# Optimization experiments

Measured on AMD Instinct MI355X. Metric: run time of the kernel, lower is better.

The kernel has to match this reference:

```python
import jax, jax.numpy as jnp
import numpy as np

B, S, D, E = 2, 2048, 1024, 16  # batch, cutoff (seq), dmodel, n_experts


def setup_inputs() -> dict:
    key = jax.random.key(0)
    k = jax.random.split(key, 6)
    scale = 1.0 / np.sqrt(D)
    return {
        "x": jax.random.normal(k[0], (B, S, D), dtype=jnp.float32),
        "gate": jax.random.normal(k[1], (D, E), dtype=jnp.float32) * scale,
        "W1": jax.random.normal(k[2], (E, D, D), dtype=jnp.float32) * scale,  # lin1: Linear(dmodel, dmodel*E), split per expert
        "b1": jnp.zeros((E, D), dtype=jnp.float32),
        "W2": jax.random.normal(k[3], (E, D, D), dtype=jnp.float32) * scale,  # lin2: Linear(dmodel*E, dmodel), split per expert
        "b2": jnp.zeros((D,), dtype=jnp.float32),
        "topk": 256,
    }


def reference(x, gate, W1, b1, W2, b2, topk):
    # Expert-choice gating: softmax over the token (cutoff) axis per expert.
    logits = jnp.einsum("bsd,de->bse", x, gate)            # (B, S, E)
    probs = jax.nn.softmax(logits, axis=1)                  # softmax over tokens
    # Each expert selects its top-k tokens.
    g, idx = jax.lax.top_k(jnp.swapaxes(probs, 1, 2), topk)  # (B, E, k)
    # Gather selected tokens: (B, E, k, D)
    xin = jnp.take_along_axis(x[:, None, :, :], idx[..., None], axis=2)
    # Per-expert 2-layer FFN (hidden size = dmodel, per width = dmodel*n_experts)
    h = jax.nn.relu(jnp.einsum("bekd,edf->bekf", xin, W1) + b1[None, :, None, :])
    out = jnp.einsum("bekf,efd->bekd", h, W2) + b2           # (B, E, k, D)
    weighted = out * g[..., None]
    # Scatter-add back to token positions.
    y = jnp.zeros_like(x)
    b_idx = jnp.arange(x.shape[0])[:, None, None]            # (B, 1, 1)
    y = y.at[b_idx, idx].add(weighted)
    return y
```

## Files before the change

### kernel.cpp

```cpp
#include <hip/hip_runtime.h>
#include <stdint.h>
#include <math.h>

constexpr int CB = 2;
constexpr int CS = 2048;
constexpr int CD = 1024;
constexpr int CE = 16;
constexpr int CK = 256;

typedef short bf16x8 __attribute__((ext_vector_type(8)));
typedef float f32x4 __attribute__((ext_vector_type(4)));

typedef __attribute__((address_space(3))) unsigned short lds_us;

__device__ __forceinline__ bf16x8 ds_read128(const lds_us* p) {
    bf16x8 v;
    asm volatile("ds_read_b128 %0, %1" : "=v"(v) : "v"(p));
    return v;
}

__device__ inline unsigned short f2bf(float f) {
    union { float f; uint32_t u; } v; v.f = f;
    uint32_t u = v.u;
    uint32_t r = (u + 0x7FFFu + ((u >> 16) & 1u)) >> 16;
    return (unsigned short)r;
}

__global__ __launch_bounds__(256)
void logits_part_kernel(const float* __restrict__ x,
                        const float* __restrict__ gate,
                        float* __restrict__ part,
                        float* __restrict__ y) {
    const int tt = blockIdx.x;
    const int dt = blockIdx.y;
    const int tid = threadIdx.x;

    {
        const int bb = dt * 16 + tt;
        float* yb = y + (size_t)bb * 16384 + tid * 4;
        const f32x4 z = {0.f, 0.f, 0.f, 0.f};
#pragma unroll
        for (int i = 0; i < 16; i++) *(f32x4*)(yb + i * 1024) = z;
    }

    __shared__ float Xs[256 * 17];

    float acc[CE];
#pragma unroll
    for (int e = 0; e < CE; e++) acc[e] = 0.0f;

    const int tokl = tid >> 2;
    const int c4 = (tid & 3) << 2;

    for (int dch = 0; dch < 4; dch++) {
        const int dbase = dt * 64 + dch * 16;
        __syncthreads();
#pragma unroll
        for (int q = 0; q < 4; q++) {
            const int tok = q * 64 + tokl;
            const f32x4 v = *(const f32x4*)(x + ((size_t)(tt * 256 + tok)) * CD + dbase + c4);
            Xs[tok * 17 + c4 + 0] = v[0];
            Xs[tok * 17 + c4 + 1] = v[1];
            Xs[tok * 17 + c4 + 2] = v[2];
            Xs[tok * 17 + c4 + 3] = v[3];
        }
        __syncthreads();
#pragma unroll
        for (int d = 0; d < 16; d++) {
            const float xv = Xs[tid * 17 + d];
            const float* gr = gate + (size_t)(dbase + d) * CE;
#pragma unroll
            for (int e = 0; e < CE; e++) acc[e] = fmaf(xv, gr[e], acc[e]);
        }
    }
    float* pr = part + ((size_t)dt * (CB * CS) + tt * 256 + tid) * CE;
#pragma unroll
    for (int e = 0; e < CE; e++) pr[e] = acc[e];
}

__global__ __launch_bounds__(256)
void logits_reduce_kernel(const float* __restrict__ part,
                          float* __restrict__ logits) {
    const int i = blockIdx.x * 256 + threadIdx.x;
    float s = 0.0f;
#pragma unroll
    for (int p = 0; p < 16; p++) s += part[(size_t)p * (CB * CS * CE) + i];
    logits[i] = s;
}

__global__ void topk_kernel(const float* __restrict__ logits,
                            int* __restrict__ idx_out,
                            float* __restrict__ g_out) {
    const int be = blockIdx.x;
    const int b = be >> 4, e = be & 15;
    const int tid = threadIdx.x;
    const int lane = tid & 63, wid = tid >> 6;

    __shared__ float redf[4];
    __shared__ int hist[256];
    __shared__ int wsum[4];
    __shared__ int sh_bin, sh_rank;
    __shared__ int scnt, eqc;
    __shared__ int eqbuf[CS];

    float lv[8], p[8];
    unsigned int uv[8];
#pragma unroll
    for (int j = 0; j < 8; j++) {
        const int s = tid + j * 256;
        lv[j] = logits[((size_t)(b * CS + s)) * CE + e];
    }
    float m = lv[0];
#pragma unroll
    for (int j = 1; j < 8; j++) m = fmaxf(m, lv[j]);
#pragma unroll
    for (int o = 32; o > 0; o >>= 1) m = fmaxf(m, __shfl_down(m, o));
    if (lane == 0) redf[wid] = m;
    __syncthreads();
    m = fmaxf(fmaxf(redf[0], redf[1]), fmaxf(redf[2], redf[3]));
    __syncthreads();
    float lsum = 0.0f;
#pragma unroll
    for (int j = 0; j < 8; j++) {
        p[j] = expf(lv[j] - m);
        uv[j] = __float_as_uint(p[j]);
        lsum += p[j];
    }
#pragma unroll
    for (int o = 32; o > 0; o >>= 1) lsum += __shfl_down(lsum, o);
    if (lane == 0) redf[wid] = lsum;
    __syncthreads();
    const float total = redf[0] + redf[1] + redf[2] + redf[3];
    const float inv_total = 1.0f / total;

    unsigned int prefix = 0;
    int kneed = CK;
    for (int pass = 0; pass < 4; pass++) {
        const int shift = 24 - 8 * pass;
        __syncthreads();
        hist[tid] = 0;
        __syncthreads();
        const unsigned int hmask = (pass == 0) ? 0u : (0xFFFFFFFFu << (shift + 8));
#pragma unroll
        for (int j = 0; j < 8; j++)
            if ((uv[j] & hmask) == prefix)
                atomicAdd(&hist[(uv[j] >> shift) & 255], 1);
        __syncthreads();
        const int own = hist[tid];
        int s = own;
#pragma unroll
        for (int o = 1; o < 64; o <<= 1) {
            int t = __shfl_down(s, o);
            if (lane + o < 64) s += t;
        }
        if (lane == 0) wsum[wid] = s;
        __syncthreads();
        int above = 0;
        for (int ww = wid + 1; ww < 4; ww++) above += wsum[ww];
        const int incl = s + above;
        if (incl >= kneed && (incl - own) < kneed) {
            sh_bin = tid;
            sh_rank = kneed - (incl - own);
        }
        __syncthreads();
        prefix |= ((unsigned int)sh_bin) << shift;
        kneed = sh_rank;
    }
    const unsigned int v = prefix;
    const int quota = kneed;

    if (tid == 0) { scnt = 0; eqc = 0; }
    __syncthreads();
#pragma unroll
    for (int j = 0; j < 8; j++) {
        const int s = tid + j * 256;
        if (uv[j] > v) {
            const int pos = atomicAdd(&scnt, 1);
            idx_out[be * CK + pos] = s;
            g_out[be * CK + pos] = p[j] * inv_total;
        } else if (uv[j] == v) {
            const int pos = atomicAdd(&eqc, 1);
            eqbuf[pos] = s;
        }
    }
    __syncthreads();
    if (tid == 0) {
        const int cgt = scnt;
        const int n = eqc;
        const float gv = __uint_as_float(v) * inv_total;
        if (n > quota) {
            for (int i = 0; i < quota; i++) {
                int mn = i;
                for (int k2 = i + 1; k2 < n; k2++)
                    if (eqbuf[k2] < eqbuf[mn]) mn = k2;
                const int t2 = eqbuf[i]; eqbuf[i] = eqbuf[mn]; eqbuf[mn] = t2;
            }
        }
        for (int i = 0; i < quota; i++) {
            idx_out[be * CK + cgt + i] = eqbuf[i];
            g_out[be * CK + cgt + i] = gv;
        }
    }
}

__device__ __forceinline__
void wt_body(const float* __restrict__ W, unsigned short* __restrict__ Wt,
             int kt, int nt, int e, int tid, unsigned short* T) {
    const float* src = W + (size_t)e * CD * CD;
    unsigned short* dst = Wt + (size_t)e * CD * CD;

    const int kr = tid >> 4;
    const int n4 = (tid & 15) << 2;
#pragma unroll
    for (int it = 0; it < 4; it++) {
        const int k = it * 16 + kr;
        const f32x4 v = *(const f32x4*)(src + (size_t)(kt * 64 + k) * CD + nt * 64 + n4);
        const int pp = k >> 4;
        const int klo = k & 15;
#pragma unroll
        for (int i = 0; i < 4; i++) {
            const int n = n4 + i;
            T[n * 64 + ((pp ^ ((n >> 2) & 3)) << 4) + klo] = f2bf(v[i]);
        }
    }
    __syncthreads();
    const int n = tid >> 2;
    const int pp = tid & 3;
    const int sw = pp ^ ((n >> 2) & 3);
    const uint4 a = *(const uint4*)&T[n * 64 + (sw << 4)];
    const uint4 b = *(const uint4*)&T[n * 64 + (sw << 4) + 8];
    unsigned short* drow = dst + (size_t)(nt * 64 + n) * CD + kt * 64 + pp * 16;
    *(uint4*)drow = a;
    *(uint4*)(drow + 8) = b;
}

__global__ __launch_bounds__(256)
void wt_kernel(const float* __restrict__ W, unsigned short* __restrict__ Wt) {
    __shared__ unsigned short T[64 * 64];
    wt_body(W, Wt, blockIdx.x, blockIdx.y, blockIdx.z, threadIdx.x, T);
}

__global__ __launch_bounds__(256)
void prep_kernel(const float* __restrict__ W1, unsigned short* __restrict__ Wt,
                 const float* __restrict__ x, const int* __restrict__ idx_ws,
                 unsigned short* __restrict__ xinbuf) {
    __shared__ unsigned short T[64 * 64];
    const int bx = blockIdx.x;
    if (bx < 4096) {
        wt_body(W1, Wt, bx & 15, (bx >> 4) & 15, bx >> 8, threadIdx.x, T);
    } else {
        const int row = bx - 4096;
        const int be = row >> 8;
        const int b = be >> 4;
        const int tok = idx_ws[row];
        const int c0 = threadIdx.x * 4;
        const f32x4 f = *(const f32x4*)(x + ((size_t)b * CS + tok) * CD + c0);
        union { unsigned short u[4]; uint2 v; } t;
        t.u[0] = f2bf(f[0]); t.u[1] = f2bf(f[1]); t.u[2] = f2bf(f[2]); t.u[3] = f2bf(f[3]);
        *(uint2*)(xinbuf + (size_t)row * CD + c0) = t.v;
    }
}

#define MFMA16(A_, B_, C_) __builtin_amdgcn_mfma_f32_16x16x32_bf16((A_), (B_), (C_), 0, 0, 0)

template <int PHASE>
__global__ __launch_bounds__(512, 1)
void ffn_gemm(const unsigned short* __restrict__ Ain,
              const unsigned short* __restrict__ Wt,
              const float* __restrict__ bias,
              unsigned short* __restrict__ hout,
              const int* __restrict__ idx_ws,
              const float* __restrict__ g_ws,
              float* __restrict__ y) {
    const int id = blockIdx.x;
    const int xcd = id & 7;
    const int q = id >> 3;
    const int e = ((q & 1) << 3) | xcd;
    const int b = (q >> 1) & 1;
    const int ntile = q >> 2;
    const int be = b * CE + e;
    const int tid = threadIdx.x;
    const int w = tid >> 6, l = tid & 63;
    const int wm = w >> 1, wn = w & 1;
    const int quad = l >> 4, lr = l & 15;

    __shared__ __align__(16) unsigned char SMEM[98304];
    unsigned short* Ar = (unsigned short*)SMEM;
    unsigned short* Aw = Ar + 16384;
    unsigned short* Br = Aw + 16384;
    unsigned short* Bw = Br + 8192;

    f32x4 acc[4][4];
    const f32x4 zz = {0.f, 0.f, 0.f, 0.f};
#pragma unroll
    for (int mi = 0; mi < 4; mi++)
#pragma unroll
        for (int ni = 0; ni < 4; ni++) acc[mi][ni] = zz;

    const unsigned short* Agb = Ain + (size_t)be * CK * CD;
    const unsigned short* Bgb = Wt + ((size_t)e * CD + ntile * 128) * CD;

    const unsigned short* pAg[4]; int dA[4];
#pragma unroll
    for (int j = 0; j < 4; j++) {
        const int u = w * 256 + j * 64 + l;
        const int row = u >> 3;
        const int c = (u & 7) ^ (row & 7);
        pAg[j] = Agb + (size_t)row * CD + c * 8;
        dA[j] = u * 8;
    }
    const unsigned short* pBg[2]; int dB[2];
#pragma unroll
    for (int j = 0; j < 2; j++) {
        const int u = w * 128 + j * 64 + l;
        const int row = u >> 3;
        const int c = (u & 7) ^ (row & 7);
        pBg[j] = Bgb + (size_t)row * CD + c * 8;
        dB[j] = u * 8;
    }

    const int sc0 = (quad ^ (lr & 7)) * 8;
    const int sc1 = sc0 ^ 32;
    int offA[2][4], offB[2][4];
#pragma unroll
    for (int mi = 0; mi < 4; mi++) {
        const int r = wm * 64 + mi * 16 + lr;
        offA[0][mi] = r * 64 + sc0;
        offA[1][mi] = r * 64 + sc1;
    }
#pragma unroll
    for (int ni = 0; ni < 4; ni++) {
        const int r = wn * 64 + ni * 16 + lr;
        offB[0][ni] = r * 64 + sc0;
        offB[1][ni] = r * 64 + sc1;
    }

    bf16x8 sA0, sA1, sA2, sA3, sB0, sB1;
    sA0 = *(const bf16x8*)(pAg[0]); sA1 = *(const bf16x8*)(pAg[1]);
    sA2 = *(const bf16x8*)(pAg[2]); sA3 = *(const bf16x8*)(pAg[3]);
    sB0 = *(const bf16x8*)(pBg[0]); sB1 = *(const bf16x8*)(pBg[1]);
    *(bf16x8*)(Ar + dA[0]) = sA0; *(bf16x8*)(Ar + dA[1]) = sA1;
    *(bf16x8*)(Ar + dA[2]) = sA2; *(bf16x8*)(Ar + dA[3]) = sA3;
    *(bf16x8*)(Br + dB[0]) = sB0; *(bf16x8*)(Br + dB[1]) = sB1;
    __syncthreads();

#pragma unroll 1
    for (int t = 0; t < 16; t++) {
        if (t < 15) {
            const int kel = (t + 1) * 64;
            sA0 = *(const bf16x8*)(pAg[0] + kel);
            sA1 = *(const bf16x8*)(pAg[1] + kel);
            sA2 = *(const bf16x8*)(pAg[2] + kel);
            sA3 = *(const bf16x8*)(pAg[3] + kel);
            sB0 = *(const bf16x8*)(pBg[0] + kel);
            sB1 = *(const bf16x8*)(pBg[1] + kel);
        }
        bf16x8 a0, a1, a2, a3, b0, b1, b2, b3;
#pragma unroll
        for (int kk = 0; kk < 2; kk++) {
            a0 = ds_read128((lds_us*)Ar + offA[kk][0]);
            a1 = ds_read128((lds_us*)Ar + offA[kk][1]);
            a2 = ds_read128((lds_us*)Ar + offA[kk][2]);
            a3 = ds_read128((lds_us*)Ar + offA[kk][3]);
            b0 = ds_read128((lds_us*)Br + offB[kk][0]);
            b1 = ds_read128((lds_us*)Br + offB[kk][1]);
            b2 = ds_read128((lds_us*)Br + offB[kk][2]);
            b3 = ds_read128((lds_us*)Br + offB[kk][3]);
            asm volatile("s_waitcnt lgkmcnt(0)"
                         : "+v"(a0), "+v"(a1), "+v"(a2), "+v"(a3),
                           "+v"(b0), "+v"(b1), "+v"(b2), "+v"(b3) :: "memory");
            __builtin_amdgcn_s_setprio(1);
            acc[0][0] = MFMA16(a0, b0, acc[0][0]);
            acc[1][0] = MFMA16(a1, b0, acc[1][0]);
            acc[2][0] = MFMA16(a2, b0, acc[2][0]);
            acc[3][0] = MFMA16(a3, b0, acc[3][0]);
            acc[0][1] = MFMA16(a0, b1, acc[0][1]);
            acc[1][1] = MFMA16(a1, b1, acc[1][1]);
            acc[2][1] = MFMA16(a2, b1, acc[2][1]);
            acc[3][1] = MFMA16(a3, b1, acc[3][1]);
            acc[0][2] = MFMA16(a0, b2, acc[0][2]);
            acc[1][2] = MFMA16(a1, b2, acc[1][2]);
            acc[2][2] = MFMA16(a2, b2, acc[2][2]);
            acc[3][2] = MFMA16(a3, b2, acc[3][2]);
            acc[0][3] = MFMA16(a0, b3, acc[0][3]);
            acc[1][3] = MFMA16(a1, b3, acc[1][3]);
            acc[2][3] = MFMA16(a2, b3, acc[2][3]);
            acc[3][3] = MFMA16(a3, b3, acc[3][3]);
            __builtin_amdgcn_s_setprio(0);
        }
        if (t < 15) {
            *(bf16x8*)(Aw + dA[0]) = sA0; *(bf16x8*)(Aw + dA[1]) = sA1;
            *(bf16x8*)(Aw + dA[2]) = sA2; *(bf16x8*)(Aw + dA[3]) = sA3;
            *(bf16x8*)(Bw + dB[0]) = sB0; *(bf16x8*)(Bw + dB[1]) = sB1;
            __syncthreads();
            unsigned short* tp = Ar; Ar = Aw; Aw = tp;
            tp = Br; Br = Bw; Bw = tp;
        }
    }

    __syncthreads();
    float* LT = (float*)SMEM;
#pragma unroll 1
    for (int h = 0; h < 2; h++) {
        if ((wm >> 1) == h) {
            const int rb = (wm & 1) * 64;
#pragma unroll
            for (int mi = 0; mi < 4; mi++)
#pragma unroll
                for (int ni = 0; ni < 4; ni++)
#pragma unroll
                    for (int r = 0; r < 4; r++)
                        LT[(rb + mi * 16 + quad * 4 + r) * 133 + wn * 64 + ni * 16 + lr] =
                            acc[mi][ni][r];
        }
        __syncthreads();
        if (PHASE == 0) {
#pragma unroll
            for (int rr = 0; rr < 4; rr++) {
                const int row = w * 16 + rr * 4 + (l >> 4);
                const int col = (l & 15) * 8;
                const int slot = h * 128 + row;
                const float* lrow = LT + row * 133 + col;
                const float* brow = bias + e * CD + ntile * 128 + col;
                union { unsigned short us[8]; uint4 v; } pk;
#pragma unroll
                for (int i = 0; i < 8; i++)
                    pk.us[i] = f2bf(fmaxf(lrow[i] + brow[i], 0.0f));
                *(uint4*)(hout + ((size_t)be * CK + slot) * CD + ntile * 128 + col) = pk.v;
            }
        } else {
#pragma unroll 1
            for (int rr = 0; rr < 16; rr++) {
                const int row = w * 16 + rr;
                const int slot = h * 128 + row;
                const int tok = idx_ws[be * CK + slot];
                const float gval = g_ws[be * CK + slot];
                float* yrow = y + ((size_t)b * CS + tok) * CD + ntile * 128;
                const float* lrow = LT + row * 133;
                const float* brow = bias + ntile * 128;
#pragma unroll
                for (int i = 0; i < 2; i++) {
                    const int col = i * 64 + l;
                    atomicAdd(&yrow[col], (lrow[col] + brow[col]) * gval);
                }
            }
        }
        __syncthreads();
    }
}

extern "C" void kernel_launch(void* const* d_in, const int* in_sizes, int n_in,
                              void* d_out, int out_size, void* d_ws, size_t ws_size,
                              hipStream_t stream) {
    const float* x    = (const float*)d_in[0];
    const float* gate = (const float*)d_in[1];
    const float* W1   = (const float*)d_in[2];
    const float* b1   = (const float*)d_in[3];
    const float* W2   = (const float*)d_in[4];
    const float* b2   = (const float*)d_in[5];
    float* y = (float*)d_out;

    char* ws = (char*)d_ws;
    float* logits = (float*)ws;
    int* idxw = (int*)(ws + 262144);
    float* gw = (float*)(ws + 294912);
    unsigned short* xinbuf = (unsigned short*)(ws + 327680);
    unsigned short* hbuf = (unsigned short*)(ws + 17104896);
    float* partbuf = (float*)(ws + 17104896);
    unsigned short* wtbuf = (unsigned short*)(ws + 33882112);

    logits_part_kernel<<<dim3(16, 16), 256, 0, stream>>>(x, gate, partbuf, y);
    logits_reduce_kernel<<<CB * CS * CE / 256, 256, 0, stream>>>(partbuf, logits);
    topk_kernel<<<CB * CE, 256, 0, stream>>>(logits, idxw, gw);
    prep_kernel<<<4096 + CB * CE * CK, 256, 0, stream>>>(W1, wtbuf, x, idxw, xinbuf);
    ffn_gemm<0><<<256, 512, 0, stream>>>(xinbuf, wtbuf, b1, hbuf, idxw, gw, y);
    wt_kernel<<<dim3(16, 16, CE), 256, 0, stream>>>(W2, wtbuf);
    ffn_gemm<1><<<256, 512, 0, stream>>>(hbuf, wtbuf, b2, nullptr, idxw, gw, y);
}
```

Baseline: 276.3 us.

## Fuse weight fp32-to-bf16 transpose into GEMM LDS staging

Removes the separate weight transpose/convert kernels and instead has each GEMM block load fp32 weights directly, convert them to bf16 and write them transposed into the swizzled LDS tile. This eliminates the write and re-read of a bf16 weight copy and two kernel launches. In exchange the GEMM main loop does twice the global bytes for weights, extra conversion ALU work, and narrower scattered LDS stores.

```diff
diff --git a/kernel.cpp b/kernel.cpp
--- a/kernel.cpp
+++ b/kernel.cpp
@@ -203,62 +203,18 @@
     }
 }
 
-__device__ __forceinline__
-void wt_body(const float* __restrict__ W, unsigned short* __restrict__ Wt,
-             int kt, int nt, int e, int tid, unsigned short* T) {
-    const float* src = W + (size_t)e * CD * CD;
-    unsigned short* dst = Wt + (size_t)e * CD * CD;
-
-    const int kr = tid >> 4;
-    const int n4 = (tid & 15) << 2;
-#pragma unroll
-    for (int it = 0; it < 4; it++) {
-        const int k = it * 16 + kr;
-        const f32x4 v = *(const f32x4*)(src + (size_t)(kt * 64 + k) * CD + nt * 64 + n4);
-        const int pp = k >> 4;
-        const int klo = k & 15;
-#pragma unroll
-        for (int i = 0; i < 4; i++) {
-            const int n = n4 + i;
-            T[n * 64 + ((pp ^ ((n >> 2) & 3)) << 4) + klo] = f2bf(v[i]);
-        }
-    }
-    __syncthreads();
-    const int n = tid >> 2;
-    const int pp = tid & 3;
-    const int sw = pp ^ ((n >> 2) & 3);
-    const uint4 a = *(const uint4*)&T[n * 64 + (sw << 4)];
-    const uint4 b = *(const uint4*)&T[n * 64 + (sw << 4) + 8];
-    unsigned short* drow = dst + (size_t)(nt * 64 + n) * CD + kt * 64 + pp * 16;
-    *(uint4*)drow = a;
-    *(uint4*)(drow + 8) = b;
-}
-
-__global__ __launch_bounds__(256)
-void wt_kernel(const float* __restrict__ W, unsigned short* __restrict__ Wt) {
-    __shared__ unsigned short T[64 * 64];
-    wt_body(W, Wt, blockIdx.x, blockIdx.y, blockIdx.z, threadIdx.x, T);
-}
-
-__global__ __launch_bounds__(256)
-void prep_kernel(const float* __restrict__ W1, unsigned short* __restrict__ Wt,
-                 const float* __restrict__ x, const int* __restrict__ idx_ws,
-                 unsigned short* __restrict__ xinbuf) {
-    __shared__ unsigned short T[64 * 64];
-    const int bx = blockIdx.x;
-    if (bx < 4096) {
-        wt_body(W1, Wt, bx & 15, (bx >> 4) & 15, bx >> 8, threadIdx.x, T);
-    } else {
-        const int row = bx - 4096;
-        const int be = row >> 8;
-        const int b = be >> 4;
-        const int tok = idx_ws[row];
-        const int c0 = threadIdx.x * 4;
-        const f32x4 f = *(const f32x4*)(x + ((size_t)b * CS + tok) * CD + c0);
-        union { unsigned short u[4]; uint2 v; } t;
-        t.u[0] = f2bf(f[0]); t.u[1] = f2bf(f[1]); t.u[2] = f2bf(f[2]); t.u[3] = f2bf(f[3]);
-        *(uint2*)(xinbuf + (size_t)row * CD + c0) = t.v;
-    }
+__global__ void gather_kernel(const float* __restrict__ x,
+                              const int* __restrict__ idx_ws,
+                              unsigned short* __restrict__ xinbuf) {
+    const int row = blockIdx.x;
+    const int be = row >> 8;
+    const int b = be >> 4;
+    const int tok = idx_ws[row];
+    const int c0 = threadIdx.x * 4;
+    const f32x4 f = *(const f32x4*)(x + ((size_t)b * CS + tok) * CD + c0);
+    union { unsigned short u[4]; uint2 v; } t;
+    t.u[0] = f2bf(f[0]); t.u[1] = f2bf(f[1]); t.u[2] = f2bf(f[2]); t.u[3] = f2bf(f[3]);
+    *(uint2*)(xinbuf + (size_t)row * CD + c0) = t.v;
 }
 
 #define MFMA16(A_, B_, C_) __builtin_amdgcn_mfma_f32_16x16x32_bf16((A_), (B_), (C_), 0, 0, 0)
@@ -266,7 +222,7 @@
 template <int PHASE>
 __global__ __launch_bounds__(512, 1)
 void ffn_gemm(const unsigned short* __restrict__ Ain,
-              const unsigned short* __restrict__ Wt,
+              const float* __restrict__ Wf,
               const float* __restrict__ bias,
               unsigned short* __restrict__ hout,
               const int* __restrict__ idx_ws,
@@ -298,7 +254,6 @@
         for (int ni = 0; ni < 4; ni++) acc[mi][ni] = zz;
 
     const unsigned short* Agb = Ain + (size_t)be * CK * CD;
-    const unsigned short* Bgb = Wt + ((size_t)e * CD + ntile * 128) * CD;
 
     const unsigned short* pAg[4]; int dA[4];
 #pragma unroll
@@ -309,14 +264,16 @@
         pAg[j] = Agb + (size_t)row * CD + c * 8;
         dA[j] = u * 8;
     }
-    const unsigned short* pBg[2]; int dB[2];
-#pragma unroll
-    for (int j = 0; j < 2; j++) {
-        const int u = w * 128 + j * 64 + l;
-        const int row = u >> 3;
-        const int c = (u & 7) ^ (row & 7);
-        pBg[j] = Bgb + (size_t)row * CD + c * 8;
-        dB[j] = u * 8;
+
+    const int kq = tid >> 5;
+    const int nq = tid & 31;
+    const float* pWg = Wf + (size_t)e * CD * CD + (size_t)(kq * 4) * CD
+                          + ntile * 128 + nq * 4;
+    int wbB[4];
+#pragma unroll
+    for (int i = 0; i < 4; i++) {
+        const int n = nq * 4 + i;
+        wbB[i] = n * 64 + (((kq >> 1) ^ (n & 7)) << 3) + (kq & 1) * 4;
     }
 
     const int sc0 = (quad ^ (lr & 7)) * 8;
@@ -335,13 +292,23 @@
         offB[1][ni] = r * 64 + sc1;
     }
 
-    bf16x8 sA0, sA1, sA2, sA3, sB0, sB1;
+    bf16x8 sA0, sA1, sA2, sA3;
+    f32x4 sW0, sW1, sW2, sW3;
     sA0 = *(const bf16x8*)(pAg[0]); sA1 = *(const bf16x8*)(pAg[1]);
     sA2 = *(const bf16x8*)(pAg[2]); sA3 = *(const bf16x8*)(pAg[3]);
-    sB0 = *(const bf16x8*)(pBg[0]); sB1 = *(const bf16x8*)(pBg[1]);
+    sW0 = *(const f32x4*)(pWg);
+    sW1 = *(const f32x4*)(pWg + CD);
+    sW2 = *(const f32x4*)(pWg + 2 * CD);
+    sW3 = *(const f32x4*)(pWg + 3 * CD);
     *(bf16x8*)(Ar + dA[0]) = sA0; *(bf16x8*)(Ar + dA[1]) = sA1;
     *(bf16x8*)(Ar + dA[2]) = sA2; *(bf16x8*)(Ar + dA[3]) = sA3;
-    *(bf16x8*)(Br + dB[0]) = sB0; *(bf16x8*)(Br + dB[1]) = sB1;
+#pragma unroll
+    for (int i = 0; i < 4; i++) {
+        union { unsigned short us[4]; uint2 v; } pk;
+        pk.us[0] = f2bf(sW0[i]); pk.us[1] = f2bf(sW1[i]);
+        pk.us[2] = f2bf(sW2[i]); pk.us[3] = f2bf(sW3[i]);
+        *(uint2*)(Br + wbB[i]) = pk.v;
+    }
     __syncthreads();
 
 #pragma unroll 1
@@ -352,8 +319,11 @@
             sA1 = *(const bf16x8*)(pAg[1] + kel);
             sA2 = *(const bf16x8*)(pAg[2] + kel);
             sA3 = *(const bf16x8*)(pAg[3] + kel);
-            sB0 = *(const bf16x8*)(pBg[0] + kel);
-            sB1 = *(const bf16x8*)(pBg[1] + kel);
+            const float* pw = pWg + (size_t)kel * CD;
+            sW0 = *(const f32x4*)(pw);
+            sW1 = *(const f32x4*)(pw + CD);
+            sW2 = *(const f32x4*)(pw + 2 * CD);
+            sW3 = *(const f32x4*)(pw + 3 * CD);
         }
         bf16x8 a0, a1, a2, a3, b0, b1, b2, b3;
 #pragma unroll
@@ -391,7 +361,13 @@
         if (t < 15) {
             *(bf16x8*)(Aw + dA[0]) = sA0; *(bf16x8*)(Aw + dA[1]) = sA1;
             *(bf16x8*)(Aw + dA[2]) = sA2; *(bf16x8*)(Aw + dA[3]) = sA3;
-            *(bf16x8*)(Bw + dB[0]) = sB0; *(bf16x8*)(Bw + dB[1]) = sB1;
+#pragma unroll
+            for (int i = 0; i < 4; i++) {
+                union { unsigned short us[4]; uint2 v; } pk;
+                pk.us[0] = f2bf(sW0[i]); pk.us[1] = f2bf(sW1[i]);
+                pk.us[2] = f2bf(sW2[i]); pk.us[3] = f2bf(sW3[i]);
+                *(uint2*)(Bw + wbB[i]) = pk.v;
+            }
             __syncthreads();
             unsigned short* tp = Ar; Ar = Aw; Aw = tp;
             tp = Br; Br = Bw; Bw = tp;
@@ -467,13 +443,11 @@
     unsigned short* xinbuf = (unsigned short*)(ws + 327680);
     unsigned short* hbuf = (unsigned short*)(ws + 17104896);
     float* partbuf = (float*)(ws + 17104896);
-    unsigned short* wtbuf = (unsigned short*)(ws + 33882112);
 
     logits_part_kernel<<<dim3(16, 16), 256, 0, stream>>>(x, gate, partbuf, y);
     logits_reduce_kernel<<<CB * CS * CE / 256, 256, 0, stream>>>(partbuf, logits);
     topk_kernel<<<CB * CE, 256, 0, stream>>>(logits, idxw, gw);
-    prep_kernel<<<4096 + CB * CE * CK, 256, 0, stream>>>(W1, wtbuf, x, idxw, xinbuf);
-    ffn_gemm<0><<<256, 512, 0, stream>>>(xinbuf, wtbuf, b1, hbuf, idxw, gw, y);
-    wt_kernel<<<dim3(16, 16, CE), 256, 0, stream>>>(W2, wtbuf);
-    ffn_gemm<1><<<256, 512, 0, stream>>>(hbuf, wtbuf, b2, nullptr, idxw, gw, y);
-}
+    gather_kernel<<<CB * CE * CK, 256, 0, stream>>>(x, idxw, xinbuf);
+    ffn_gemm<0><<<256, 512, 0, stream>>>(xinbuf, W1, b1, hbuf, idxw, gw, y);
+    ffn_gemm<1><<<256, 512, 0, stream>>>(hbuf, W2, b2, nullptr, idxw, gw, y);
+}
```

Result: faster. 265.5 us (-3.9%).
